# Performance work log

Hardware: AMD Instinct MI355X
Metric: run time of the kernel (lower is better)

Reference implementation:

```python
import jax, jax.numpy as jnp
import numpy as np

B, S, H = 2, 2048, 2048
NQ, NKV, DH = 16, 8, 128
EPS = 1e-6
ROPE_BASE = 10000.0


def setup_inputs() -> dict:
    key = jax.random.key(0)
    ks = jax.random.split(key, 6)
    hidden_states = jax.random.normal(ks[0], (B, S, H), dtype=jnp.float32)
    # real RoPE tables
    inv_freq = 1.0 / (ROPE_BASE ** (jnp.arange(0, DH, 2, dtype=jnp.float32) / DH))
    pos = jnp.arange(S, dtype=jnp.float32)
    freqs = pos[:, None] * inv_freq[None, :]              # [S, DH/2]
    emb = jnp.concatenate([freqs, freqs], axis=-1)        # [S, DH]
    cos = jnp.broadcast_to(jnp.cos(emb)[None], (B, S, DH))
    sin = jnp.broadcast_to(jnp.sin(emb)[None], (B, S, DH))
    # additive causal mask [1,1,S,S]
    causal = jnp.tril(jnp.ones((S, S), dtype=bool))
    attention_mask = jnp.where(causal, 0.0, jnp.finfo(jnp.float32).min)[None, None]
    q_w = jax.random.normal(ks[1], (H, H), dtype=jnp.float32) * 0.02
    k_w = jax.random.normal(ks[2], (NKV * DH, H), dtype=jnp.float32) * 0.02
    v_w = jax.random.normal(ks[3], (NKV * DH, H), dtype=jnp.float32) * 0.02
    o_w = jax.random.normal(ks[4], (H, H), dtype=jnp.float32) * 0.02
    return {"hidden_states": hidden_states, "cos": cos, "sin": sin,
            "attention_mask": attention_mask,
            "q_w": q_w, "k_w": k_w, "v_w": v_w, "o_w": o_w}


def _rotate_half(x):
    x1, x2 = jnp.split(x, 2, axis=-1)
    return jnp.concatenate([-x2, x1], axis=-1)


def _l2norm(x, eps=EPS):
    # weightless RMS norm over head_dim (Llama4TextL2Norm)
    return x * jax.lax.rsqrt(jnp.mean(x * x, axis=-1, keepdims=True) + eps)


def reference(hidden_states, cos, sin, attention_mask, q_w, k_w, v_w, o_w):
    b, s, _ = hidden_states.shape
    # projections (no bias) -> [B, n_heads, S, DH]
    q = jnp.einsum('bsh,dh->bsd', hidden_states, q_w).reshape(b, s, NQ, DH).transpose(0, 2, 1, 3)
    k = jnp.einsum('bsh,dh->bsd', hidden_states, k_w).reshape(b, s, NKV, DH).transpose(0, 2, 1, 3)
    v = jnp.einsum('bsh,dh->bsd', hidden_states, v_w).reshape(b, s, NKV, DH).transpose(0, 2, 1, 3)
    # NanoChat negates sin before standard HF rotary
    sin_e = (-sin)[:, None, :, :]   # [B,1,S,DH]
    cos_e = cos[:, None, :, :]
    q = q * cos_e + _rotate_half(q) * sin_e
    k = k * cos_e + _rotate_half(k) * sin_e
    # weightless QK RMS norm
    q = _l2norm(q)
    k = _l2norm(k)
    # GQA: repeat kv heads
    groups = NQ // NKV
    k = jnp.repeat(k, groups, axis=1)
    v = jnp.repeat(v, groups, axis=1)
    scaling = DH ** -0.5
    scores = jnp.einsum('bhqd,bhkd->bhqk', q, k) * scaling + attention_mask
    probs = jax.nn.softmax(scores, axis=-1)
    attn = jnp.einsum('bhqk,bhkd->bhqd', probs, v)           # [B,H,S,DH]
    attn = attn.transpose(0, 2, 1, 3).reshape(b, s, NQ * DH)
    out = jnp.einsum('bsd,hd->bsh', attn, o_w)
    return out
```

## Files before the change

### kernel.cpp

```cpp
#include <hip/hip_runtime.h>

typedef unsigned short ushort_t;
typedef __bf16 bf16x8 __attribute__((ext_vector_type(8)));
typedef float f32x4 __attribute__((ext_vector_type(4)));
typedef unsigned int u32x4 __attribute__((ext_vector_type(4)));
typedef unsigned short us4 __attribute__((ext_vector_type(4)));
typedef unsigned short us8 __attribute__((ext_vector_type(8)));

#define DEVINL __device__ __forceinline__

DEVINL ushort_t f2bf(float f) {
    unsigned u = __float_as_uint(f);
    u += 0x7FFF + ((u >> 16) & 1);
    return (ushort_t)(u >> 16);
}
DEVINL float bf2f(ushort_t h) { return __uint_as_float(((unsigned)h) << 16); }

DEVINL void gload_lds16(const void* g, void* l) {
    __builtin_amdgcn_global_load_lds(
        (const __attribute__((address_space(1))) void*)g,
        (__attribute__((address_space(3))) void*)l, 16, 0, 0);
}

DEVINL bf16x8 ld_frag(const ushort_t* p) {
    us8 v = *(const us8*)p;
    return __builtin_bit_cast(bf16x8, v);
}

#define BARRIER_KEEP4()  asm volatile("s_waitcnt vmcnt(4)\n\ts_barrier" ::: "memory")
#define BARRIER_KEEP8()  asm volatile("s_waitcnt vmcnt(8)\n\ts_barrier" ::: "memory")
#define BARRIER_KEEP0()  asm volatile("s_waitcnt vmcnt(0)\n\ts_barrier" ::: "memory")

__global__ __launch_bounds__(256) void convert_all(const f32x4* __restrict__ h,
                                                   const f32x4* __restrict__ qw,
                                                   const f32x4* __restrict__ kw,
                                                   const f32x4* __restrict__ vw,
                                                   const f32x4* __restrict__ ow,
                                                   us4* __restrict__ hb,
                                                   us4* __restrict__ wqkv,
                                                   us4* __restrict__ owb) {
    const int N0 = 2097152;
    const int N1 = 1048576;
    const int N2 = 524288;
    const int N3 = 524288;
    int i = blockIdx.x * 256 + threadIdx.x;
    const f32x4* src; us4* dst;
    if (i < N0)                               { src = h  + i;                 dst = hb + i; }
    else if ((i -= N0) < N1)                  { src = qw + i;                 dst = wqkv + i; }
    else if ((i -= N1) < N2)                  { src = kw + i;                 dst = wqkv + 1048576 + i; }
    else if ((i -= N2) < N3)                  { src = vw + i;                 dst = wqkv + 1572864 + i; }
    else                                      { i -= N3; src = ow + i;       dst = owb + i; }
    f32x4 f = *src;
    us4 o;
    o[0] = f2bf(f[0]); o[1] = f2bf(f[1]); o[2] = f2bf(f[2]); o[3] = f2bf(f[3]);
    *dst = o;
}

template <typename OutT>
__global__ __launch_bounds__(256) void gemm_bt(const ushort_t* __restrict__ A,
                                               const ushort_t* __restrict__ W,
                                               OutT* __restrict__ C,
                                               int M, int N, int K) {
    __shared__ ushort_t As[3][128 * 32];
    __shared__ ushort_t Bs[3][128 * 32];
    const int t = threadIdx.x;
    const int w = t >> 6, lane = t & 63;
    const int quad = lane >> 4, l16 = lane & 15;
    const int sw = (l16 >> 1) & 3;
    const int lid = blockIdx.x;
    const int xcd = lid & 7, j = lid >> 3;
    const int r = j & 15, st = j >> 4;
    const int bm = (xcd * 4 + (r & 3)) * 128;
    const int bn = (st * 4 + (r >> 2)) * 128;
    const int wr = (w >> 1) * 64, wc = (w & 1) * 64;

    f32x4 acc[4][4];
#pragma unroll
    for (int i = 0; i < 4; i++)
#pragma unroll
        for (int jj = 0; jj < 4; jj++) acc[i][jj] = f32x4{0.f, 0.f, 0.f, 0.f};

    auto stage = [&](int k0, int buf) {
#pragma unroll
        for (int i = 0; i < 2; i++) {
            int u = i * 256 + t;
            int row = u >> 2;
            int ce = ((u & 3) ^ ((row >> 1) & 3)) * 8;
            gload_lds16(A + (size_t)(bm + row) * K + k0 + ce, (char*)As[buf] + u * 16);
            gload_lds16(W + (size_t)(bn + row) * K + k0 + ce, (char*)Bs[buf] + u * 16);
        }
    };

    const int NIT = K >> 5;
    stage(0, 0);
    stage(32, 1);
    int cb = 0, pb = 2;
    for (int n = 0; n < NIT; ++n) {
        if (n + 1 < NIT) BARRIER_KEEP4();
        else             BARRIER_KEEP0();
        if (n + 2 < NIT) stage((n + 2) * 32, pb);
        const ushort_t* Ab = As[cb];
        const ushort_t* Bb = Bs[cb];
        cb = cb == 2 ? 0 : cb + 1;
        pb = pb == 2 ? 0 : pb + 1;
        bf16x8 af[4], bf[4];
#pragma unroll
        for (int mt = 0; mt < 4; mt++)
            af[mt] = ld_frag(&Ab[(wr + mt * 16 + l16) * 32 + (quad ^ sw) * 8]);
#pragma unroll
        for (int nt = 0; nt < 4; nt++)
            bf[nt] = ld_frag(&Bb[(wc + nt * 16 + l16) * 32 + (quad ^ sw) * 8]);
#pragma unroll
        for (int mt = 0; mt < 4; mt++)
#pragma unroll
            for (int nt = 0; nt < 4; nt++)
                acc[mt][nt] = __builtin_amdgcn_mfma_f32_16x16x32_bf16(af[mt], bf[nt],
                                                                      acc[mt][nt], 0, 0, 0);
    }

#pragma unroll
    for (int mt = 0; mt < 4; mt++)
#pragma unroll
        for (int nt = 0; nt < 4; nt++) {
            int row = bm + wr + mt * 16 + quad * 4;
            int col = bn + wc + nt * 16 + l16;
#pragma unroll
            for (int rr = 0; rr < 4; rr++) {
                float v = acc[mt][nt][rr];
                if constexpr (sizeof(OutT) == 2)
                    C[(size_t)(row + rr) * N + col] = (OutT)f2bf(v);
                else
                    C[(size_t)(row + rr) * N + col] = v;
            }
        }
}

__global__ __launch_bounds__(256) void rope_norm(const ushort_t* __restrict__ qkv,
                                                 const float* __restrict__ cosb,
                                                 const float* __restrict__ sinb,
                                                 ushort_t* __restrict__ q,
                                                 ushort_t* __restrict__ k) {
    int row = blockIdx.x;
    int b = row >> 11, s = row & 2047;
    int w = threadIdx.x >> 6, lane = threadIdx.x & 63;
    int hh = blockIdx.y * 4 + w;
    const ushort_t* src = qkv + (size_t)row * 4096 + hh * 128;
    float x1 = bf2f(src[lane]);
    float x2 = bf2f(src[lane + 64]);
    float c = cosb[(size_t)row * 128 + lane];
    float sn = sinb[(size_t)row * 128 + lane];
    float y1 = x1 * c + x2 * sn;
    float y2 = x2 * c - x1 * sn;
    float ss = y1 * y1 + y2 * y2;
#pragma unroll
    for (int off = 1; off < 64; off <<= 1) ss += __shfl_xor(ss, off);
    float rinv = rsqrtf(ss * (1.0f / 128.0f) + 1e-6f);
    y1 *= rinv; y2 *= rinv;
    ushort_t* dst;
    if (hh < 16) dst = q + (((size_t)(b * 16 + hh)) * 2048 + s) * 128;
    else         dst = k + (((size_t)(b * 8 + hh - 16)) * 2048 + s) * 128;
    dst[lane] = f2bf(y1);
    dst[lane + 64] = f2bf(y2);
}

__global__ __launch_bounds__(256) void v_transpose(const ushort_t* __restrict__ qkv,
                                                   ushort_t* __restrict__ vt) {
    __shared__ ushort_t tile[64 * 72];
    int t = threadIdx.x;
    int s0 = blockIdx.x * 64, d0 = blockIdx.y * 64, bh = blockIdx.z;
    int b = bh >> 3, kvh = bh & 7;
    {
        int sl = t >> 2, c = t & 3;
        const ushort_t* src = qkv + (size_t)(b * 2048 + s0 + sl) * 4096 + 3072 + kvh * 128 + d0 + c * 16;
        u32x4 v0 = *(const u32x4*)src;
        u32x4 v1 = *(const u32x4*)(src + 8);
        *(u32x4*)&tile[sl * 72 + c * 16] = v0;
        *(u32x4*)&tile[sl * 72 + c * 16 + 8] = v1;
    }
    __syncthreads();
    {
        int dl = t >> 2, c = t & 3;
        alignas(16) ushort_t tmp[16];
#pragma unroll
        for (int i = 0; i < 16; i++) tmp[i] = tile[(c * 16 + i) * 72 + dl];
        ushort_t* dst = vt + (size_t)(bh * 128 + d0 + dl) * 2048 + s0 + c * 16;
        *(u32x4*)dst = *(const u32x4*)&tmp[0];
        *(u32x4*)(dst + 8) = *(const u32x4*)&tmp[8];
    }
}

__global__ __launch_bounds__(256) void flash_attn(const ushort_t* __restrict__ q,
                                                  const ushort_t* __restrict__ k,
                                                  const ushort_t* __restrict__ vt,
                                                  ushort_t* __restrict__ attn) {
    __shared__ ushort_t Ks[3][4 * 64 * 32];
    __shared__ ushort_t Vts[3][2 * 128 * 32];
    __shared__ ushort_t Ps[4 * 32 * 72];
    const int t = threadIdx.x;
    const int w = t >> 6, lane = t & 63;
    const int quad = lane >> 4, l16 = lane & 15;
    const int sw = (l16 >> 1) & 3;
    const int lid = blockIdx.x;
    const int xcd = lid & 7, jj = lid >> 3;
    const int g = xcd * 2 + (jj >> 4);
    const int p = jj & 15;
    const int b = g >> 3, kvh = g & 7;
    const int h0 = kvh * 2;
    const size_t kbase = ((size_t)(b * 8 + kvh)) * 2048 * 128;
    const size_t vbase = ((size_t)(b * 8 + kvh)) * 128 * 2048;

    const float C1 = 0.12751744f;
    const float C2 = 1.45f;

    auto stage = [&](int j0, int buf) {
#pragma unroll
        for (int i = 0; i < 4; i++) {
            int u = i * 256 + t;
            int qd = u >> 8, rr = (u >> 2) & 63;
            int c4 = ((u & 3) ^ ((rr >> 1) & 3)) * 8;
            gload_lds16(k + kbase + (size_t)(j0 + rr) * 128 + qd * 32 + c4,
                        (char*)Ks[buf] + u * 16);
        }
#pragma unroll
        for (int i = 0; i < 4; i++) {
            int u = i * 256 + t;
            int ks = u >> 9, dd = (u >> 2) & 127;
            int c4 = ((u & 3) ^ ((dd >> 1) & 3)) * 8;
            gload_lds16(vt + vbase + (size_t)dd * 2048 + j0 + ks * 32 + c4,
                        (char*)Vts[buf] + u * 16);
        }
    };

    const int qtile0 = 31 - p;
    const int S_total = qtile0 + 1 + p + 1;
    auto j0_of = [&](int s) { return (s <= qtile0 ? s : s - qtile0 - 1) * 64; };

    stage(j0_of(0), 0);
    stage(j0_of(1), 1);
    int sidx = 0, cb = 0, pb = 2;

    for (int pass = 0; pass < 2; ++pass) {
        const int qi = pass ? p : qtile0;
        const int q0 = qi * 64;

        bf16x8 qf[2][4];
#pragma unroll
        for (int h = 0; h < 2; h++) {
            const size_t qbase = ((size_t)(b * 16 + h0 + h) * 2048 + q0 + w * 16 + l16) * 128;
#pragma unroll
            for (int qd = 0; qd < 4; qd++) {
                us8 v = *(const us8*)(q + qbase + qd * 32 + quad * 8);
                qf[h][qd] = __builtin_bit_cast(bf16x8, v);
            }
        }

        f32x4 o[2][8];
#pragma unroll
        for (int h = 0; h < 2; h++)
#pragma unroll
            for (int i = 0; i < 8; i++) o[h][i] = f32x4{0.f, 0.f, 0.f, 0.f};
        float lsum[2][4];
#pragma unroll
        for (int h = 0; h < 2; h++)
#pragma unroll
            for (int r = 0; r < 4; r++) lsum[h][r] = 0.f;

        for (int jt = 0; jt <= qi; ++jt) {
            const int j0 = jt * 64;
            const bool diag = (jt == qi);
            if (sidx + 1 < S_total) BARRIER_KEEP8();
            else                    BARRIER_KEEP0();
            if (sidx + 2 < S_total) stage(j0_of(sidx + 2), pb);
            const ushort_t* Kb = Ks[cb];
            const ushort_t* Vb = Vts[cb];
            cb = cb == 2 ? 0 : cb + 1;
            pb = pb == 2 ? 0 : pb + 1;
            sidx++;

            f32x4 sc[2][4];
#pragma unroll
            for (int h = 0; h < 2; h++)
#pragma unroll
                for (int c = 0; c < 4; c++) sc[h][c] = f32x4{0.f, 0.f, 0.f, 0.f};
#pragma unroll
            for (int c = 0; c < 4; c++)
#pragma unroll
                for (int qd = 0; qd < 4; qd++) {
                    bf16x8 kf = ld_frag(&Kb[qd * 2048 + (c * 16 + l16) * 32 + (quad ^ sw) * 8]);
                    sc[0][c] = __builtin_amdgcn_mfma_f32_16x16x32_bf16(qf[0][qd], kf, sc[0][c], 0, 0, 0);
                    sc[1][c] = __builtin_amdgcn_mfma_f32_16x16x32_bf16(qf[1][qd], kf, sc[1][c], 0, 0, 0);
                }

#pragma unroll
            for (int c = 0; c < 4; c++)
#pragma unroll
                for (int r = 0; r < 4; r++) {
                    float p0 = __builtin_amdgcn_exp2f(sc[0][c][r] * C1 - C2);
                    float p1 = __builtin_amdgcn_exp2f(sc[1][c][r] * C1 - C2);
                    if (diag) {
                        int kg = j0 + c * 16 + l16;
                        int qg = q0 + w * 16 + quad * 4 + r;
                        if (kg > qg) { p0 = 0.f; p1 = 0.f; }
                    }
                    lsum[0][r] += p0;
                    lsum[1][r] += p1;
                    Ps[w * 2304 + (quad * 4 + r) * 72 + c * 16 + l16] = f2bf(p0);
                    Ps[w * 2304 + (16 + quad * 4 + r) * 72 + c * 16 + l16] = f2bf(p1);
                }

#pragma unroll
            for (int ks = 0; ks < 2; ks++) {
                bf16x8 pf0 = ld_frag(&Ps[w * 2304 + l16 * 72 + ks * 32 + quad * 8]);
                bf16x8 pf1 = ld_frag(&Ps[w * 2304 + (16 + l16) * 72 + ks * 32 + quad * 8]);
#pragma unroll
                for (int od = 0; od < 8; od++) {
                    bf16x8 vf = ld_frag(&Vb[ks * 4096 + (od * 16 + l16) * 32 + (quad ^ sw) * 8]);
                    o[0][od] = __builtin_amdgcn_mfma_f32_16x16x32_bf16(pf0, vf, o[0][od], 0, 0, 0);
                    o[1][od] = __builtin_amdgcn_mfma_f32_16x16x32_bf16(pf1, vf, o[1][od], 0, 0, 0);
                }
            }
        }

        float rl[2][4];
#pragma unroll
        for (int h = 0; h < 2; h++)
#pragma unroll
            for (int r = 0; r < 4; r++) {
                float s = lsum[h][r];
#pragma unroll
                for (int off = 1; off < 16; off <<= 1) s += __shfl_xor(s, off);
                rl[h][r] = 1.0f / s;
            }
#pragma unroll
        for (int h = 0; h < 2; h++) {
            const size_t obase = ((size_t)(b * 2048 + q0 + w * 16 + quad * 4)) * 2048 + (h0 + h) * 128;
#pragma unroll
            for (int od = 0; od < 8; od++)
#pragma unroll
                for (int r = 0; r < 4; r++)
                    attn[obase + (size_t)r * 2048 + od * 16 + l16] = f2bf(o[h][od][r] * rl[h][r]);
        }
    }
}

extern "C" void kernel_launch(void* const* d_in, const int* in_sizes, int n_in,
                              void* d_out, int out_size, void* d_ws, size_t ws_size,
                              hipStream_t stream) {
    (void)in_sizes; (void)n_in; (void)out_size; (void)ws_size;
    const float* hidden = (const float*)d_in[0];
    const float* cosb   = (const float*)d_in[1];
    const float* sinb   = (const float*)d_in[2];
    const float* q_w    = (const float*)d_in[4];
    const float* k_w    = (const float*)d_in[5];
    const float* v_w    = (const float*)d_in[6];
    const float* o_w    = (const float*)d_in[7];

    char* ws = (char*)d_ws;
    ushort_t* hb   = (ushort_t*)(ws);
    ushort_t* wqkv = (ushort_t*)(ws + (16ull << 20));
    ushort_t* owb  = (ushort_t*)(ws + (32ull << 20));
    ushort_t* qkv  = (ushort_t*)(ws + (40ull << 20));
    ushort_t* attn = qkv;
    ushort_t* qb   = (ushort_t*)(ws + (72ull << 20));
    ushort_t* kb   = (ushort_t*)(ws + (88ull << 20));
    ushort_t* vt   = (ushort_t*)(ws + (96ull << 20));

    convert_all<<<20480, 256, 0, stream>>>((const f32x4*)hidden, (const f32x4*)q_w,
                                           (const f32x4*)k_w, (const f32x4*)v_w,
                                           (const f32x4*)o_w,
                                           (us4*)hb, (us4*)wqkv, (us4*)owb);

    gemm_bt<ushort_t><<<1024, 256, 0, stream>>>(hb, wqkv, qkv, 4096, 4096, 2048);
    rope_norm<<<dim3(4096, 6), 256, 0, stream>>>(qkv, cosb, sinb, qb, kb);
    v_transpose<<<dim3(32, 2, 16), 256, 0, stream>>>(qkv, vt);
    flash_attn<<<256, 256, 0, stream>>>(qb, kb, vt, attn);
    gemm_bt<float><<<512, 256, 0, stream>>>(attn, owb, (float*)d_out, 4096, 2048, 2048);
}
```

Measured before the change: 372.7 us.

## Replace GEMM with 256x256-tile 8-wave ping-pong kernel with priority scheduling

Swaps the 128x128-tile, 4-wave, 3-stage GEMM for a 256x256-tile, 512-thread kernel with K=64 steps and two LDS buffers. Each K step splits into four MFMA quadrants, with async global-to-LDS loads for the next tiles placed between them and s_setprio raised around MFMA bursts, so loads overlap compute. The larger tiles raise arithmetic intensity and cut global traffic per FLOP. The output-projection GEMM now launches only 128 blocks, fewer than the CU count, and the 128KB LDS footprint limits occupancy to one block per CU.

```diff
diff --git a/kernel.cpp b/kernel.cpp
--- a/kernel.cpp
+++ b/kernel.cpp
@@ -26,6 +26,10 @@
     us8 v = *(const us8*)p;
     return __builtin_bit_cast(bf16x8, v);
 }
+
+#define BAR()     asm volatile("s_barrier" ::: "memory")
+#define LGKM0()   asm volatile("s_waitcnt lgkmcnt(0)" ::: "memory")
+#define VMCNT(n)  asm volatile("s_waitcnt vmcnt(" #n ")" ::: "memory")
 
 #define BARRIER_KEEP4()  asm volatile("s_waitcnt vmcnt(4)\n\ts_barrier" ::: "memory")
 #define BARRIER_KEEP8()  asm volatile("s_waitcnt vmcnt(8)\n\ts_barrier" ::: "memory")
@@ -57,76 +61,143 @@
 }
 
 template <typename OutT>
-__global__ __launch_bounds__(256) void gemm_bt(const ushort_t* __restrict__ A,
-                                               const ushort_t* __restrict__ W,
-                                               OutT* __restrict__ C,
-                                               int M, int N, int K) {
-    __shared__ ushort_t As[3][128 * 32];
-    __shared__ ushort_t Bs[3][128 * 32];
+__global__ __launch_bounds__(512, 2) void gemm256(const ushort_t* __restrict__ A,
+                                                  const ushort_t* __restrict__ W,
+                                                  OutT* __restrict__ C,
+                                                  int N, int K) {
+    __shared__ ushort_t As[2][256 * 64];
+    __shared__ ushort_t Bs[2][256 * 64];
     const int t = threadIdx.x;
-    const int w = t >> 6, lane = t & 63;
+    const int lane = t & 63;
     const int quad = lane >> 4, l16 = lane & 15;
-    const int sw = (l16 >> 1) & 3;
-    const int lid = blockIdx.x;
-    const int xcd = lid & 7, j = lid >> 3;
-    const int r = j & 15, st = j >> 4;
-    const int bm = (xcd * 4 + (r & 3)) * 128;
-    const int bn = (st * 4 + (r >> 2)) * 128;
-    const int wr = (w >> 1) * 64, wc = (w & 1) * 64;
-
-    f32x4 acc[4][4];
-#pragma unroll
-    for (int i = 0; i < 4; i++)
+    const int wm = t >> 8, wn = (t >> 6) & 3;
+
+    int bid = blockIdx.x;
+    int xcd = bid & 7, j = bid >> 3;
+    int tm, tn;
+    if (N == 4096) { tm = (xcd >> 1) * 4 + (j >> 3); tn = (xcd & 1) * 8 + (j & 7); }
+    else           { tm = xcd * 2 + (j >> 3);        tn = j & 7; }
+    const int bm = tm * 256, bn = tn * 256;
+
+    const int srow0 = t >> 3;
+    const int sg0 = ((t & 7) ^ (srow0 & 7)) * 8;
+    const int srow1 = srow0 + 64;
+    const int sg1 = ((t & 7) ^ (srow1 & 7)) * 8;
+
+    auto stageA = [&](int buf, int half, int k0) {
+        gload_lds16(A + (size_t)(bm + half * 128 + srow0) * K + k0 + sg0,
+                    &As[buf][half * 8192 + t * 8]);
+        gload_lds16(A + (size_t)(bm + half * 128 + srow1) * K + k0 + sg1,
+                    &As[buf][half * 8192 + 4096 + t * 8]);
+    };
+    auto stageB = [&](int buf, int half, int k0) {
+        gload_lds16(W + (size_t)(bn + half * 128 + srow0) * K + k0 + sg0,
+                    &Bs[buf][half * 8192 + t * 8]);
+        gload_lds16(W + (size_t)(bn + half * 128 + srow1) * K + k0 + sg1,
+                    &Bs[buf][half * 8192 + 4096 + t * 8]);
+    };
+
+    const int xsw = l16 & 7;
+    const int arow = (wm * 128 + l16) * 64;
+    const int brow = (wn * 64 + l16) * 64;
+    const int ac0 = ((0 + quad) ^ xsw) * 8;
+    const int ac1 = ((4 + quad) ^ xsw) * 8;
+
+    auto ldA = [&](int buf, int mf, int kk) {
+        return ld_frag(&As[buf][arow + mf * 1024 + (kk ? ac1 : ac0)]);
+    };
+    auto ldB = [&](int buf, int nf, int kk) {
+        return ld_frag(&Bs[buf][brow + nf * 1024 + (kk ? ac1 : ac0)]);
+    };
+
+    f32x4 acc[8][4];
+#pragma unroll
+    for (int i = 0; i < 8; i++)
 #pragma unroll
         for (int jj = 0; jj < 4; jj++) acc[i][jj] = f32x4{0.f, 0.f, 0.f, 0.f};
 
-    auto stage = [&](int k0, int buf) {
-#pragma unroll
-        for (int i = 0; i < 2; i++) {
-            int u = i * 256 + t;
-            int row = u >> 2;
-            int ce = ((u & 3) ^ ((row >> 1) & 3)) * 8;
-            gload_lds16(A + (size_t)(bm + row) * K + k0 + ce, (char*)As[buf] + u * 16);
-            gload_lds16(W + (size_t)(bn + row) * K + k0 + ce, (char*)Bs[buf] + u * 16);
-        }
-    };
-
-    const int NIT = K >> 5;
-    stage(0, 0);
-    stage(32, 1);
-    int cb = 0, pb = 2;
-    for (int n = 0; n < NIT; ++n) {
-        if (n + 1 < NIT) BARRIER_KEEP4();
-        else             BARRIER_KEEP0();
-        if (n + 2 < NIT) stage((n + 2) * 32, pb);
-        const ushort_t* Ab = As[cb];
-        const ushort_t* Bb = Bs[cb];
-        cb = cb == 2 ? 0 : cb + 1;
-        pb = pb == 2 ? 0 : pb + 1;
-        bf16x8 af[4], bf[4];
+    const int NIT = K >> 6;
+    stageA(0, 0, 0); stageA(0, 1, 0); stageB(0, 0, 0); stageB(0, 1, 0);
+    VMCNT(4);
+    stageB(1, 0, 64); stageB(1, 1, 64); stageA(1, 0, 64);
+    VMCNT(6);
+    BAR();
+
+    bf16x8 a[4][2], b[4][2];
+    for (int tt = 0; tt < NIT; ++tt) {
+        const int buf = tt & 1;
+        const int k2 = (tt + 2) << 6;
+
+#pragma unroll
+        for (int mt = 0; mt < 4; mt++) { a[mt][0] = ldA(buf, mt, 0); a[mt][1] = ldA(buf, mt, 1); }
+#pragma unroll
+        for (int nt = 0; nt < 4; nt++) { b[nt][0] = ldB(buf, nt, 0); b[nt][1] = ldB(buf, nt, 1); }
+        if (tt + 1 < NIT) stageA(buf ^ 1, 1, (tt + 1) << 6);
+        BAR(); LGKM0();
+        __builtin_amdgcn_s_setprio(1);
 #pragma unroll
         for (int mt = 0; mt < 4; mt++)
-            af[mt] = ld_frag(&Ab[(wr + mt * 16 + l16) * 32 + (quad ^ sw) * 8]);
-#pragma unroll
-        for (int nt = 0; nt < 4; nt++)
-            bf[nt] = ld_frag(&Bb[(wc + nt * 16 + l16) * 32 + (quad ^ sw) * 8]);
+#pragma unroll
+            for (int nt = 0; nt < 2; nt++)
+#pragma unroll
+                for (int kk = 0; kk < 2; kk++)
+                    acc[mt][nt] = __builtin_amdgcn_mfma_f32_16x16x32_bf16(a[mt][kk], b[nt][kk], acc[mt][nt], 0, 0, 0);
+        __builtin_amdgcn_s_setprio(0);
+        LGKM0();
+        BAR();
+
+        if (tt + 2 < NIT) stageB(buf, 0, k2);
+        BAR();
+        __builtin_amdgcn_s_setprio(1);
 #pragma unroll
         for (int mt = 0; mt < 4; mt++)
 #pragma unroll
-            for (int nt = 0; nt < 4; nt++)
-                acc[mt][nt] = __builtin_amdgcn_mfma_f32_16x16x32_bf16(af[mt], bf[nt],
-                                                                      acc[mt][nt], 0, 0, 0);
+            for (int nt = 0; nt < 2; nt++)
+#pragma unroll
+                for (int kk = 0; kk < 2; kk++)
+                    acc[mt][2 + nt] = __builtin_amdgcn_mfma_f32_16x16x32_bf16(a[mt][kk], b[2 + nt][kk], acc[mt][2 + nt], 0, 0, 0);
+        __builtin_amdgcn_s_setprio(0);
+        BAR();
+
+#pragma unroll
+        for (int mt = 0; mt < 4; mt++) { a[mt][0] = ldA(buf, 4 + mt, 0); a[mt][1] = ldA(buf, 4 + mt, 1); }
+        if (tt + 2 < NIT) stageB(buf, 1, k2);
+        BAR(); LGKM0();
+        __builtin_amdgcn_s_setprio(1);
+#pragma unroll
+        for (int mt = 0; mt < 4; mt++)
+#pragma unroll
+            for (int nt = 0; nt < 2; nt++)
+#pragma unroll
+                for (int kk = 0; kk < 2; kk++)
+                    acc[4 + mt][nt] = __builtin_amdgcn_mfma_f32_16x16x32_bf16(a[mt][kk], b[nt][kk], acc[4 + mt][nt], 0, 0, 0);
+        __builtin_amdgcn_s_setprio(0);
+        BAR();
+
+        if (tt + 2 < NIT)      { stageA(buf, 0, k2); VMCNT(6); }
+        else if (tt + 1 < NIT) { VMCNT(0); }
+        BAR();
+        __builtin_amdgcn_s_setprio(1);
+#pragma unroll
+        for (int mt = 0; mt < 4; mt++)
+#pragma unroll
+            for (int nt = 0; nt < 2; nt++)
+#pragma unroll
+                for (int kk = 0; kk < 2; kk++)
+                    acc[4 + mt][2 + nt] = __builtin_amdgcn_mfma_f32_16x16x32_bf16(a[mt][kk], b[2 + nt][kk], acc[4 + mt][2 + nt], 0, 0, 0);
+        __builtin_amdgcn_s_setprio(0);
+        BAR();
     }
 
 #pragma unroll
-    for (int mt = 0; mt < 4; mt++)
-#pragma unroll
-        for (int nt = 0; nt < 4; nt++) {
-            int row = bm + wr + mt * 16 + quad * 4;
-            int col = bn + wc + nt * 16 + l16;
+    for (int mf = 0; mf < 8; mf++)
+#pragma unroll
+        for (int nf = 0; nf < 4; nf++) {
+            const int row = bm + wm * 128 + mf * 16 + quad * 4;
+            const int col = bn + wn * 64 + nf * 16 + l16;
 #pragma unroll
             for (int rr = 0; rr < 4; rr++) {
-                float v = acc[mt][nt][rr];
+                float v = acc[mf][nf][rr];
                 if constexpr (sizeof(OutT) == 2)
                     C[(size_t)(row + rr) * N + col] = (OutT)f2bf(v);
                 else
@@ -370,9 +441,9 @@
                                            (const f32x4*)o_w,
                                            (us4*)hb, (us4*)wqkv, (us4*)owb);
 
-    gemm_bt<ushort_t><<<1024, 256, 0, stream>>>(hb, wqkv, qkv, 4096, 4096, 2048);
+    gemm256<ushort_t><<<256, 512, 0, stream>>>(hb, wqkv, qkv, 4096, 2048);
     rope_norm<<<dim3(4096, 6), 256, 0, stream>>>(qkv, cosb, sinb, qb, kb);
     v_transpose<<<dim3(32, 2, 16), 256, 0, stream>>>(qkv, vt);
     flash_attn<<<256, 256, 0, stream>>>(qb, kb, vt, attn);
-    gemm_bt<float><<<512, 256, 0, stream>>>(attn, owb, (float*)d_out, 4096, 2048, 2048);
-}
+    gemm256<float><<<128, 512, 0, stream>>>(attn, owb, (float*)d_out, 2048, 2048);
+}
```

New measurement: 352.9 us. 5.3% less time.
